# Kernel tuning notes

Measured on AMD Instinct MI355X. Metric: run time of the kernel, lower is better.

Reference implementation:

```python
import jax, jax.numpy as jnp
import numpy as np

H_IMG = 64; W_IMG = 64; N = H_IMG * W_IMG
IN_CH = 128; HID = 8; HEADS = 4; OUT_CH = 64; BATCH = 16
NEG_SLOPE = 0.2


def _build_graph():
    # Faithful replication of GATHead._construct_graph (n_neighbor=3 -> 5x5 unfold windows)
    m = np.arange(N).reshape(H_IMG, W_IMG)
    pad = np.full((H_IMG + 6, W_IMG + 6), -1, dtype=np.int64)
    pad[3:3 + H_IMG, 3:3 + W_IMG] = m
    win = np.lib.stride_tricks.sliding_window_view(pad, (5, 5))  # (h+2, w+2, 5, 5)
    lookup = win.reshape(-1, 25)[:N]                             # first N rows used
    adj = np.zeros((N, N), dtype=bool)
    rows = np.repeat(np.arange(N), 25)
    cols = lookup.reshape(-1)
    valid = cols >= 0
    adj[rows[valid], cols[valid]] = True
    adj = adj | adj.T                       # dgl.to_bidirected (simple graph)
    u, v = np.nonzero(adj)
    src = np.concatenate([u, np.arange(N)]).astype(np.int32)  # dgl.add_self_loop appends (i,i)
    dst = np.concatenate([v, np.arange(N)]).astype(np.int32)
    return src, dst


def setup_inputs() -> dict:
    key = jax.random.key(0)
    ks = jax.random.split(key, 9)
    src, dst = _build_graph()
    s = 0.1
    return {
        "x": jax.random.normal(ks[0], (BATCH, IN_CH, H_IMG, W_IMG), jnp.float32),
        "W1": jax.random.normal(ks[1], (IN_CH, HEADS * HID), jnp.float32) * s,
        "al1": jax.random.normal(ks[2], (1, HEADS, HID), jnp.float32) * s,
        "ar1": jax.random.normal(ks[3], (1, HEADS, HID), jnp.float32) * s,
        "b1": jax.random.normal(ks[4], (HEADS * HID,), jnp.float32) * s,
        "W2": jax.random.normal(ks[5], (HEADS * HID, OUT_CH), jnp.float32) * s,
        "al2": jax.random.normal(ks[6], (1, 1, OUT_CH), jnp.float32) * s,
        "ar2": jax.random.normal(ks[7], (1, 1, OUT_CH), jnp.float32) * s,
        "b2": jax.random.normal(ks[8], (OUT_CH,), jnp.float32) * s,
        "src": jnp.asarray(src),
        "dst": jnp.asarray(dst),
    }


def _gat_conv(x, W, al, ar, b, src, dst, heads, dout):
    # DGL GATConv: linear proj, per-edge LeakyReLU attention logits, per-dst edge softmax, scatter-sum
    feat = (x @ W).reshape(-1, heads, dout)          # (N, H, D)
    el = jnp.sum(feat * al, axis=-1)                 # (N, H)
    er = jnp.sum(feat * ar, axis=-1)                 # (N, H)
    e = jax.nn.leaky_relu(el[src] + er[dst], NEG_SLOPE)  # (E, H)
    emax = jax.ops.segment_max(e, dst, num_segments=N)
    ex = jnp.exp(e - emax[dst])
    denom = jax.ops.segment_sum(ex, dst, num_segments=N)
    a = ex / denom[dst]                              # (E, H) edge-softmax coeffs
    out = jax.ops.segment_sum(a[:, :, None] * feat[src], dst, num_segments=N)  # (N, H, D)
    return out + b.reshape(1, heads, dout)


def _mish(x):
    return x * jnp.tanh(jax.nn.softplus(x))


def reference(x, W1, al1, ar1, b1, W2, al2, ar2, b2, src, dst):
    xb = x.reshape(BATCH, IN_CH, N).transpose(0, 2, 1)  # b c h w -> b (h w) c

    def single(xi):
        h = _gat_conv(xi, W1, al1, ar1, b1, src, dst, HEADS, HID)   # (N, 4, 8)
        h = _mish(h).reshape(N, HEADS * HID)                        # merge 'n c heads -> n (c heads)'
        return _gat_conv(h, W2, al2, ar2, b2, src, dst, 1, OUT_CH)  # (N, 1, OUT_CH)

    out = jax.vmap(single)(xb)                                      # (B, N, 1, OUT_CH)
    # readout: b (h w) d1 d2 -> b (d1 d2) h w
    return out.reshape(BATCH, H_IMG, W_IMG, OUT_CH).transpose(0, 3, 1, 2)
```

## Files before the change

### kernel.cpp

```cpp
#include <hip/hip_runtime.h>
#include <hip/hip_bf16.h>

#define N_NODES 4096
#define BATCH 16
#define IN_CH 128
#define HID 8
#define HEADS 4
#define F1 (HEADS*HID)
#define OUT_CH 64
#define MAXD 64

__device__ __forceinline__ int node_swz(int bid) {
    return (bid & 7) * 512 + (bid >> 3);
}

__global__ void k_init(int* cursor, int* nbrp) {
    int i = blockIdx.x * 256 + threadIdx.x;
    if (i < N_NODES * MAXD) nbrp[i] = i >> 6;
    if (i < N_NODES) cursor[i] = 0;
}

__global__ void k_fill(const int* __restrict__ srcA, const int* __restrict__ dstA, int E,
                       int* cursor, int* nbrp) {
    int e = blockIdx.x * 256 + threadIdx.x;
    if (e < E) {
        int n = dstA[e];
        int pos = atomicAdd(&cursor[n], 1);
        nbrp[(n << 6) + pos] = srcA[e];
    }
}

__global__ __launch_bounds__(256) void k_feat1(const float* __restrict__ x,
                                               const float* __restrict__ W1,
                                               const float* __restrict__ al1,
                                               const float* __restrict__ ar1,
                                               float* __restrict__ feat1,
                                               float* __restrict__ el1,
                                               float* __restrict__ er1) {
    __shared__ float lW1[IN_CH * F1];
    __shared__ float lal[F1], lar[F1];
    __shared__ float lt[64 * 33];
    __shared__ float lel[64 * 4], ler[64 * 4];
    int t = threadIdx.x;
    for (int i = t; i < IN_CH * F1; i += 256) lW1[i] = W1[i];
    if (t < F1) { lal[t] = al1[t]; lar[t] = ar1[t]; }
    __syncthreads();

    int b = blockIdx.y;
    int n0 = blockIdx.x * 64;
    int q = t >> 6;
    int nl = t & 63;
    int n = n0 + nl;
    const float* xp = x + (size_t)b * (IN_CH * N_NODES) + n;
    const float* wq = lW1 + q * HID;

    float acc[HID];
    #pragma unroll
    for (int i = 0; i < HID; i++) acc[i] = 0.f;
    #pragma unroll 4
    for (int c = 0; c < IN_CH; c++) {
        float xv = xp[(size_t)c * N_NODES];
        #pragma unroll
        for (int i = 0; i < HID; i++) acc[i] += xv * wq[c * F1 + i];
    }

    float el = 0.f, er = 0.f;
    #pragma unroll
    for (int i = 0; i < HID; i++) {
        el += acc[i] * lal[q * HID + i];
        er += acc[i] * lar[q * HID + i];
    }
    lel[nl * 4 + q] = el;
    ler[nl * 4 + q] = er;

    #pragma unroll
    for (int i = 0; i < HID; i++) lt[nl * 33 + q * HID + i] = acc[i];
    __syncthreads();

    float* fp = feat1 + (size_t)n0 * (BATCH * F1) + b * F1;
    #pragma unroll
    for (int k = 0; k < 8; k++) {
        int idx = k * 256 + t;
        int nn = idx >> 5, f = idx & 31;
        fp[nn * (BATCH * F1) + f] = lt[nn * 33 + f];
    }
    if (t < 64) {
        ((float4*)el1)[(n0 + t) * BATCH + b] = *(float4*)&lel[t * 4];
        ((float4*)er1)[(n0 + t) * BATCH + b] = *(float4*)&ler[t * 4];
    }
}

__global__ __launch_bounds__(256) void k_gat1(const float* __restrict__ feat1,
                                              const float* __restrict__ el1,
                                              const float* __restrict__ er1,
                                              const int* __restrict__ nbrp,
                                              const int* __restrict__ deg,
                                              const float* __restrict__ b1v,
                                              float* __restrict__ h1) {
    int t = threadIdx.x;
    int n = node_swz(blockIdx.x);
    int f2 = t & 15;
    int eoff = ((t >> 4) << 2) + (f2 >> 2);
    int dg = deg[n];
    const int* nb = nbrp + (n << 6);
    float ern = er1[(n << 6) + eoff];
    int t2 = t << 1;

    float ax = 0.f, ay = 0.f, wsum = 0.f;
    for (int g = 0; g < MAXD / 4; g++) {
        if (g * 4 >= dg) break;
        #pragma unroll
        for (int u = 0; u < 4; u++) {
            int j = g * 4 + u;
            int s = nb[j];
            float e = el1[(s << 6) + eoff] + ern;
            e = (e > 0.f) ? e : 0.2f * e;
            float w = (j < dg) ? __expf(e) : 0.f;
            wsum += w;
            float2 f = *(const float2*)&feat1[(s << 9) + t2];
            ax += w * f.x; ay += w * f.y;
        }
    }
    float inv = 1.f / wsum;
    float2 bb = *(const float2*)&b1v[f2 * 2];
    float v0 = ax * inv + bb.x;
    float v1 = ay * inv + bb.y;
    float e0 = __expf(v0), e1 = __expf(v1);
    float p0 = e0 * (e0 + 2.f), p1 = e1 * (e1 + 2.f);
    float2 o = { v0 * p0 / (p0 + 2.f), v1 * p1 / (p1 + 2.f) };
    *(float2*)&h1[(n << 9) + t2] = o;
}

__global__ __launch_bounds__(256) void k_feat2(const float* __restrict__ h1,
                                               const float* __restrict__ W2,
                                               const float* __restrict__ al2,
                                               const float* __restrict__ ar2,
                                               float* __restrict__ feat2,
                                               float* __restrict__ el2,
                                               float* __restrict__ er2) {
    __shared__ float lW2[F1 * OUT_CH];
    __shared__ float lh[BATCH * F1];
    __shared__ float lae[2 * OUT_CH];
    int t = threadIdx.x;
    int n = node_swz(blockIdx.x);
    for (int i = t; i < F1 * OUT_CH; i += 256) lW2[i] = W2[i];
    if (t < OUT_CH) { lae[t] = al2[t]; lae[OUT_CH + t] = ar2[t]; }
    *(float2*)&lh[t * 2] = *(const float2*)&h1[(n << 9) + t * 2];
    __syncthreads();

    int b = t >> 4, c4 = t & 15;
    float hreg[F1];
    #pragma unroll
    for (int k = 0; k < F1; k++) hreg[k] = lh[b * F1 + k];
    float4 acc = {0.f, 0.f, 0.f, 0.f};
    #pragma unroll
    for (int k = 0; k < F1; k++) {
        float4 w = *(float4*)&lW2[k * OUT_CH + c4 * 4];
        acc.x += hreg[k] * w.x; acc.y += hreg[k] * w.y;
        acc.z += hreg[k] * w.z; acc.w += hreg[k] * w.w;
    }
    *(float4*)&feat2[(n << 10) + (t << 2)] = acc;

    float4 a4 = *(float4*)&lae[c4 * 4];
    float4 r4 = *(float4*)&lae[OUT_CH + c4 * 4];
    float pl = acc.x * a4.x + acc.y * a4.y + acc.z * a4.z + acc.w * a4.w;
    float pr = acc.x * r4.x + acc.y * r4.y + acc.z * r4.z + acc.w * r4.w;
    #pragma unroll
    for (int off = 1; off < 16; off <<= 1) {
        pl += __shfl_xor(pl, off, 64);
        pr += __shfl_xor(pr, off, 64);
    }
    if (c4 == 0) { el2[n * BATCH + b] = pl; er2[n * BATCH + b] = pr; }
}

__global__ __launch_bounds__(256) void k_gat2(const float* __restrict__ feat2,
                                              const float* __restrict__ el2,
                                              const float* __restrict__ er2,
                                              const int* __restrict__ nbrp,
                                              const int* __restrict__ deg,
                                              const float* __restrict__ b2v,
                                              float* __restrict__ out2) {
    int t = threadIdx.x;
    int n = node_swz(blockIdx.x);
    int b = t >> 4, c4 = t & 15;
    int dg = deg[n];
    const int* nb = nbrp + (n << 6);
    float ern = er2[n * BATCH + b];
    int t4 = t << 2;

    float4 acc = {0.f, 0.f, 0.f, 0.f};
    float den = 0.f;
    for (int g = 0; g < MAXD / 4; g++) {
        if (g * 4 >= dg) break;
        #pragma unroll
        for (int u = 0; u < 4; u++) {
            int j = g * 4 + u;
            int s = nb[j];
            float e = el2[(s << 4) + b] + ern;
            e = (e > 0.f) ? e : 0.2f * e;
            float w = (j < dg) ? __expf(e) : 0.f;
            den += w;
            float4 f = *(const float4*)&feat2[(s << 10) + t4];
            acc.x += w * f.x; acc.y += w * f.y; acc.z += w * f.z; acc.w += w * f.w;
        }
    }
    float inv = 1.f / den;
    float4 bb = *(const float4*)&b2v[c4 * 4];
    float4 o = { acc.x * inv + bb.x, acc.y * inv + bb.y,
                 acc.z * inv + bb.z, acc.w * inv + bb.w };
    *(float4*)&out2[(n << 10) + t4] = o;
}

__global__ __launch_bounds__(256) void k_trans(const float* __restrict__ out2,
                                               float* __restrict__ out) {
    __shared__ float tile[64][65];
    int t = threadIdx.x;
    int b = blockIdx.y;
    int n0 = blockIdx.x * 64;
    int i = t >> 2;
    int c0 = (t & 3) * 4;
    #pragma unroll
    for (int p = 0; p < 4; p++) {
        int c = c0 + p * 16;
        float4 v = *(const float4*)&out2[(size_t)(n0 + i) * (BATCH * OUT_CH) + b * OUT_CH + c];
        tile[i][c] = v.x; tile[i][c + 1] = v.y; tile[i][c + 2] = v.z; tile[i][c + 3] = v.w;
    }
    __syncthreads();
    int nl = t & 63;
    int cw = t >> 6;
    #pragma unroll
    for (int q = 0; q < 16; q++) {
        int c = q * 4 + cw;
        out[(size_t)(b * OUT_CH + c) * N_NODES + n0 + nl] = tile[nl][c];
    }
}

extern "C" void kernel_launch(void* const* d_in, const int* in_sizes, int n_in,
                              void* d_out, int out_size, void* d_ws, size_t ws_size,
                              hipStream_t stream) {
    const float* x   = (const float*)d_in[0];
    const float* W1  = (const float*)d_in[1];
    const float* al1 = (const float*)d_in[2];
    const float* ar1 = (const float*)d_in[3];
    const float* b1v = (const float*)d_in[4];
    const float* W2  = (const float*)d_in[5];
    const float* al2 = (const float*)d_in[6];
    const float* ar2 = (const float*)d_in[7];
    const float* b2v = (const float*)d_in[8];
    const int* srcA  = (const int*)d_in[9];
    const int* dstA  = (const int*)d_in[10];
    int E = in_sizes[9];

    char* ws = (char*)d_ws;
    int*   cursor = (int*)(ws);
    int*   nbrp   = (int*)(ws + 16384);
    float* feat1  = (float*)(ws + 1064960);
    float* el1    = (float*)(ws + 9453568);
    float* er1    = (float*)(ws + 10502144);
    float* h1     = (float*)(ws + 11550720);
    float* feat2  = (float*)(ws + 19939328);
    float* el2    = (float*)(ws + 36716544);
    float* er2    = (float*)(ws + 36978688);
    float* out2   = feat1;

    float* out = (float*)d_out;
    dim3 blk(256);

    k_init<<<dim3((N_NODES * MAXD + 255) / 256), blk, 0, stream>>>(cursor, nbrp);
    k_fill<<<dim3((E + 255) / 256), blk, 0, stream>>>(srcA, dstA, E, cursor, nbrp);

    k_feat1<<<dim3(N_NODES / 64, BATCH), blk, 0, stream>>>(x, W1, al1, ar1, feat1, el1, er1);
    k_gat1 <<<dim3(N_NODES), blk, 0, stream>>>(feat1, el1, er1, nbrp, cursor, b1v, h1);

    k_feat2<<<dim3(N_NODES), blk, 0, stream>>>(h1, W2, al2, ar2, feat2, el2, er2);
    k_gat2 <<<dim3(N_NODES), blk, 0, stream>>>(feat2, el2, er2, nbrp, cursor, b2v, out2);

    k_trans<<<dim3(N_NODES / 64, BATCH), blk, 0, stream>>>(out2, out);
}
```

Baseline: 218.8 us.

## Fuse layer-1 aggregation with layer-2 projection and precompute edge weights in LDS

Merges the layer-1 GAT aggregation with the layer-2 linear projection into one kernel, so the h1 intermediate no longer makes a round trip through global memory. Both aggregation kernels now compute all LeakyReLU+exp attention weights for a node's neighbour slots once, cooperatively, into shared memory. Previously each thread recomputed them redundantly for its features. The neighbour loop is unrolled by 8. In exchange the weights are computed for all 64 padded slots even when the degree is lower, and the fused kernel uses more shared memory, which may reduce occupancy.

```diff
diff --git a/kernel.cpp b/kernel.cpp
--- a/kernel.cpp
+++ b/kernel.cpp
@@ -90,74 +90,79 @@
     }
 }
 
-__global__ __launch_bounds__(256) void k_gat1(const float* __restrict__ feat1,
-                                              const float* __restrict__ el1,
-                                              const float* __restrict__ er1,
-                                              const int* __restrict__ nbrp,
-                                              const int* __restrict__ deg,
-                                              const float* __restrict__ b1v,
-                                              float* __restrict__ h1) {
-    int t = threadIdx.x;
-    int n = node_swz(blockIdx.x);
-    int f2 = t & 15;
-    int eoff = ((t >> 4) << 2) + (f2 >> 2);
-    int dg = deg[n];
-    const int* nb = nbrp + (n << 6);
-    float ern = er1[(n << 6) + eoff];
-    int t2 = t << 1;
-
-    float ax = 0.f, ay = 0.f, wsum = 0.f;
-    for (int g = 0; g < MAXD / 4; g++) {
-        if (g * 4 >= dg) break;
-        #pragma unroll
-        for (int u = 0; u < 4; u++) {
-            int j = g * 4 + u;
-            int s = nb[j];
-            float e = el1[(s << 6) + eoff] + ern;
-            e = (e > 0.f) ? e : 0.2f * e;
-            float w = (j < dg) ? __expf(e) : 0.f;
-            wsum += w;
-            float2 f = *(const float2*)&feat1[(s << 9) + t2];
-            ax += w * f.x; ay += w * f.y;
-        }
-    }
-    float inv = 1.f / wsum;
-    float2 bb = *(const float2*)&b1v[f2 * 2];
-    float v0 = ax * inv + bb.x;
-    float v1 = ay * inv + bb.y;
-    float e0 = __expf(v0), e1 = __expf(v1);
-    float p0 = e0 * (e0 + 2.f), p1 = e1 * (e1 + 2.f);
-    float2 o = { v0 * p0 / (p0 + 2.f), v1 * p1 / (p1 + 2.f) };
-    *(float2*)&h1[(n << 9) + t2] = o;
-}
-
-__global__ __launch_bounds__(256) void k_feat2(const float* __restrict__ h1,
+__global__ __launch_bounds__(256) void k_gat1f(const float* __restrict__ feat1,
+                                               const float* __restrict__ el1,
+                                               const float* __restrict__ er1,
+                                               const int* __restrict__ nbrp,
+                                               const int* __restrict__ deg,
+                                               const float* __restrict__ b1v,
                                                const float* __restrict__ W2,
                                                const float* __restrict__ al2,
                                                const float* __restrict__ ar2,
                                                float* __restrict__ feat2,
                                                float* __restrict__ el2,
                                                float* __restrict__ er2) {
+    __shared__ float lw[MAXD * 64];
     __shared__ float lW2[F1 * OUT_CH];
     __shared__ float lh[BATCH * F1];
     __shared__ float lae[2 * OUT_CH];
+    __shared__ float lb1[F1];
     int t = threadIdx.x;
     int n = node_swz(blockIdx.x);
     for (int i = t; i < F1 * OUT_CH; i += 256) lW2[i] = W2[i];
-    if (t < OUT_CH) { lae[t] = al2[t]; lae[OUT_CH + t] = ar2[t]; }
-    *(float2*)&lh[t * 2] = *(const float2*)&h1[(n << 9) + t * 2];
-    __syncthreads();
-
-    int b = t >> 4, c4 = t & 15;
+    if (t < 2 * OUT_CH) lae[t] = (t < OUT_CH) ? al2[t] : ar2[t - OUT_CH];
+    if (t < F1) lb1[t] = b1v[t];
+
+    int dg = deg[n];
+    const int* nb = nbrp + (n << 6);
+
+    float ern = er1[(n << 6) + (t & 63)];
+    #pragma unroll
+    for (int r = 0; r < 16; r++) {
+        int idx = r * 256 + t;
+        int j = idx >> 6;
+        int s = nb[j];
+        float e = el1[(s << 6) + (idx & 63)] + ern;
+        e = (e > 0.f) ? e : 0.2f * e;
+        lw[idx] = (j < dg) ? __expf(e) : 0.f;
+    }
+    __syncthreads();
+
+    int b = t >> 4, c2 = t & 15;
+    int woff = (b << 2) + (c2 >> 2);
+    int t2 = t << 1;
+    float ax = 0.f, ay = 0.f, wsum = 0.f;
+    for (int g = 0; g < MAXD / 8; g++) {
+        if (g * 8 >= dg) break;
+        #pragma unroll
+        for (int u = 0; u < 8; u++) {
+            int j = g * 8 + u;
+            int s = nb[j];
+            float w = lw[(j << 6) + woff];
+            wsum += w;
+            float2 f = *(const float2*)&feat1[(s << 9) + t2];
+            ax += w * f.x; ay += w * f.y;
+        }
+    }
+    float inv = 1.f / wsum;
+    float v0 = ax * inv + lb1[c2 * 2];
+    float v1 = ay * inv + lb1[c2 * 2 + 1];
+    float e0 = __expf(v0), e1 = __expf(v1);
+    float p0 = e0 * (e0 + 2.f), p1 = e1 * (e1 + 2.f);
+    lh[b * F1 + c2 * 2]     = v0 * p0 / (p0 + 2.f);
+    lh[b * F1 + c2 * 2 + 1] = v1 * p1 / (p1 + 2.f);
+    __syncthreads();
+
+    int c4 = t & 15;
     float hreg[F1];
     #pragma unroll
     for (int k = 0; k < F1; k++) hreg[k] = lh[b * F1 + k];
     float4 acc = {0.f, 0.f, 0.f, 0.f};
     #pragma unroll
     for (int k = 0; k < F1; k++) {
-        float4 w = *(float4*)&lW2[k * OUT_CH + c4 * 4];
-        acc.x += hreg[k] * w.x; acc.y += hreg[k] * w.y;
-        acc.z += hreg[k] * w.z; acc.w += hreg[k] * w.w;
+        float4 w4 = *(float4*)&lW2[k * OUT_CH + c4 * 4];
+        acc.x += hreg[k] * w4.x; acc.y += hreg[k] * w4.y;
+        acc.z += hreg[k] * w4.z; acc.w += hreg[k] * w4.w;
     }
     *(float4*)&feat2[(n << 10) + (t << 2)] = acc;
 
@@ -170,7 +175,7 @@
         pl += __shfl_xor(pl, off, 64);
         pr += __shfl_xor(pr, off, 64);
     }
-    if (c4 == 0) { el2[n * BATCH + b] = pl; er2[n * BATCH + b] = pr; }
+    if (c4 == 0) { el2[(n << 4) + b] = pl; er2[(n << 4) + b] = pr; }
 }
 
 __global__ __launch_bounds__(256) void k_gat2(const float* __restrict__ feat2,
@@ -180,25 +185,35 @@
                                               const int* __restrict__ deg,
                                               const float* __restrict__ b2v,
                                               float* __restrict__ out2) {
+    __shared__ float lw2[MAXD * BATCH];
     int t = threadIdx.x;
     int n = node_swz(blockIdx.x);
-    int b = t >> 4, c4 = t & 15;
     int dg = deg[n];
     const int* nb = nbrp + (n << 6);
-    float ern = er2[n * BATCH + b];
+
+    float ern = er2[(n << 4) + (t & 15)];
+    #pragma unroll
+    for (int r = 0; r < 4; r++) {
+        int idx = r * 256 + t;
+        int j = idx >> 4;
+        int s = nb[j];
+        float e = el2[(s << 4) + (idx & 15)] + ern;
+        e = (e > 0.f) ? e : 0.2f * e;
+        lw2[idx] = (j < dg) ? __expf(e) : 0.f;
+    }
+    __syncthreads();
+
+    int b = t >> 4, c4 = t & 15;
     int t4 = t << 2;
-
     float4 acc = {0.f, 0.f, 0.f, 0.f};
     float den = 0.f;
-    for (int g = 0; g < MAXD / 4; g++) {
-        if (g * 4 >= dg) break;
+    for (int g = 0; g < MAXD / 8; g++) {
+        if (g * 8 >= dg) break;
         #pragma unroll
-        for (int u = 0; u < 4; u++) {
-            int j = g * 4 + u;
+        for (int u = 0; u < 8; u++) {
+            int j = g * 8 + u;
             int s = nb[j];
-            float e = el2[(s << 4) + b] + ern;
-            e = (e > 0.f) ? e : 0.2f * e;
-            float w = (j < dg) ? __expf(e) : 0.f;
+            float w = lw2[(j << 4) + b];
             den += w;
             float4 f = *(const float4*)&feat2[(s << 10) + t4];
             acc.x += w * f.x; acc.y += w * f.y; acc.z += w * f.z; acc.w += w * f.w;
@@ -257,7 +272,6 @@
     float* feat1  = (float*)(ws + 1064960);
     float* el1    = (float*)(ws + 9453568);
     float* er1    = (float*)(ws + 10502144);
-    float* h1     = (float*)(ws + 11550720);
     float* feat2  = (float*)(ws + 19939328);
     float* el2    = (float*)(ws + 36716544);
     float* er2    = (float*)(ws + 36978688);
@@ -270,9 +284,9 @@
     k_fill<<<dim3((E + 255) / 256), blk, 0, stream>>>(srcA, dstA, E, cursor, nbrp);
 
     k_feat1<<<dim3(N_NODES / 64, BATCH), blk, 0, stream>>>(x, W1, al1, ar1, feat1, el1, er1);
-    k_gat1 <<<dim3(N_NODES), blk, 0, stream>>>(feat1, el1, er1, nbrp, cursor, b1v, h1);
-
-    k_feat2<<<dim3(N_NODES), blk, 0, stream>>>(h1, W2, al2, ar2, feat2, el2, er2);
+    k_gat1f<<<dim3(N_NODES), blk, 0, stream>>>(feat1, el1, er1, nbrp, cursor, b1v,
+                                               W2, al2, ar2, feat2, el2, er2);
+
     k_gat2 <<<dim3(N_NODES), blk, 0, stream>>>(feat2, el2, er2, nbrp, cursor, b2v, out2);
 
     k_trans<<<dim3(N_NODES / 64, BATCH), blk, 0, stream>>>(out2, out);
```

Result: faster. 211.4 us (-3.4%).
